# Optimization experiments

Hardware: AMD Instinct MI355X
Metric: run time of the kernel (lower is better)

The kernel has to match this reference:

```python
import jax, jax.numpy as jnp
import numpy as np

L = 256  # hardcoded heatmap size in the original module
EPS = 1e-6
SIGMA = 1.0 / 3.0
BOX_T = 0.5
MASK_T = 0.1


def _gen_mask(Yp):
    """Faithful vectorized version of get_box_pos + make_heatmap for one [L,L] map."""
    M = jnp.where(Yp > BOX_T, Yp, 0.0)
    rows = jnp.sum(M, axis=1) > 0  # scan over rows (dim 0)
    cols = jnp.sum(M, axis=0) > 0  # scan over cols (dim 1)
    left = jnp.argmax(rows)                 # first nonzero row
    right = jnp.argmax(rows[::-1])          # offset of last nonzero row from the end
    up = jnp.argmax(cols)                   # first nonzero col
    down = jnp.argmax(cols[::-1])           # offset of last nonzero col from the end
    x_r = (right - left) // 2
    y_r = (down - up) // 2
    gt0 = (left + x_r).astype(jnp.float32)  # compared against coord0 = column index y
    gt1 = (up + y_r).astype(jnp.float32)    # compared against coord1 = row index x
    # make_heatmap: heatmap[x, y, :] = [y, x]
    ys = jnp.arange(L, dtype=jnp.float32)[None, :]  # coord0 over columns
    xs = jnp.arange(L, dtype=jnp.float32)[:, None]  # coord1 over rows
    d0 = (ys - gt0) / x_r.astype(jnp.float32)
    d1 = (xs - gt1) / y_r.astype(jnp.float32)
    h = d0 ** 4 + d1 ** 4                  # ((v^2)^2 summed over last dim)
    h = jnp.exp(-h / (2.0 * SIGMA) ** 2)
    return (h > MASK_T).astype(Yp.dtype)


def _per_sample(Yp, Yg):
    gen = _gen_mask(Yp)
    use_gt = jnp.max(Yg) > 0
    Yg_eff = jnp.where(use_gt, Yg, gen)
    positive = jnp.sum(Yg_eff * Yp)
    negative = jnp.sum((1.0 - Yg_eff) * Yp)
    return negative / (positive + EPS)


def setup_inputs() -> dict:
    key = jax.random.key(0)
    k1, k2, k3 = jax.random.split(key, 3)
    B = 512
    # predictions: background in [0, 0.4), a bright blob > 0.5 so box-finding works
    Y_pred = jax.random.uniform(k1, (B, L, L), dtype=jnp.float32) * 0.4
    blob = 0.6 + 0.4 * jax.random.uniform(k3, (B, 40, 80), dtype=jnp.float32)
    Y_pred = Y_pred.at[:, 100:140, 80:160].set(blob)
    # binary gt masks; zero out first half of batch to trigger the generated-mask branch
    Y_gt = (jax.random.uniform(k2, (B, L, L)) > 0.95).astype(jnp.float32)
    Y_gt = Y_gt.at[: B // 2].set(0.0)
    return {"Y_pred": Y_pred, "Y_gt": Y_gt}


def reference(Y_pred, Y_gt):
    ratios = jax.vmap(_per_sample)(Y_pred, Y_gt)  # [B]
    total = jnp.sum(ratios)
    N = Y_gt.shape[0]
    return jnp.where(total == 0, 0.0, jnp.log(total) / N)
```

## Files before the change

### kernel.cpp

```cpp
#include <hip/hip_runtime.h>
#include <math.h>

constexpr int L = 256;
constexpr float EPS = 1e-6f;
constexpr int SPLIT = 8;
constexpr int REC_WORDS = 8;


__device__ inline float wave_sum(float v) {
#pragma unroll
    for (int off = 32; off > 0; off >>= 1) v += __shfl_down(v, off, 64);
    return v;
}
__device__ inline int wave_min(int v) {
#pragma unroll
    for (int off = 32; off > 0; off >>= 1) v = min(v, __shfl_down(v, off, 64));
    return v;
}
__device__ inline int wave_max(int v) {
#pragma unroll
    for (int off = 32; off > 0; off >>= 1) v = max(v, __shfl_down(v, off, 64));
    return v;
}

__global__ __launch_bounds__(256) void init_kernel(unsigned* __restrict__ w, int n) {
    const int i = blockIdx.x * 256 + threadIdx.x;
    if (i < n) {
        const int k = i & 7;
        unsigned v = 0u;
        if (k == 3 || k == 5) v = 0x7FFFFFFFu;
        else if (k == 4 || k == 6) v = 0xFFFFFFFFu;
        w[i] = v;
    }
}

__global__ __launch_bounds__(256) void pass1_kernel(
    const float* __restrict__ Yp, const float* __restrict__ Yg,
    unsigned* __restrict__ recs) {
    const int b = blockIdx.x >> 3;
    const int s = blockIdx.x & 7;
    const int t = threadIdx.x;
    const float4* yp4 = (const float4*)(Yp + (size_t)b * L * L) + s * 2048;
    const float4* yg4 = (const float4*)(Yg + (size_t)b * L * L) + s * 2048;
    unsigned* rec = recs + b * REC_WORDS;

    float4 P[8], G[8];
#pragma unroll
    for (int k = 0; k < 8; ++k) P[k] = yp4[t + (k << 8)];
#pragma unroll
    for (int k = 0; k < 8; ++k) G[k] = yg4[t + (k << 8)];

    const int rowbase = s * 32 + (t >> 6);
    const int c0 = (t & 63) << 2;

    float sum_p = 0.f, sum_pg = 0.f;
    int anyg = 0;
    unsigned rowbits = 0u;
    unsigned cb0 = 0, cb1 = 0, cb2 = 0, cb3 = 0;
#pragma unroll
    for (int k = 0; k < 8; ++k) {
        const float4 p = P[k], g = G[k];
        sum_p  += (p.x + p.y) + (p.z + p.w);
        sum_pg += p.x * g.x + p.y * g.y + p.z * g.z + p.w * g.w;
        anyg |= (g.x > 0.f) | (g.y > 0.f) | (g.z > 0.f) | (g.w > 0.f);
        const unsigned bx = p.x > 0.5f, by = p.y > 0.5f,
                       bz = p.z > 0.5f, bw = p.w > 0.5f;
        rowbits |= (bx | by | bz | bw) << k;
        cb0 |= bx; cb1 |= by; cb2 |= bz; cb3 |= bw;
    }
    int minr = 0x7FFFFFFF, maxr = -1, minc = 0x7FFFFFFF, maxc = -1;
    if (rowbits) {
        minr = rowbase + 4 * __builtin_ctz(rowbits);
        maxr = rowbase + 4 * (31 - __builtin_clz(rowbits));
        const unsigned colbits = cb0 | (cb1 << 1) | (cb2 << 2) | (cb3 << 3);
        minc = c0 + __builtin_ctz(colbits);
        maxc = c0 + (31 - __builtin_clz(colbits));
    }

    const int wave = t >> 6, lane = t & 63;
    const float wsp = wave_sum(sum_p);
    const float wspg = wave_sum(sum_pg);
    const int wanyg = __any(anyg);
    const int wminr = wave_min(minr), wmaxr = wave_max(maxr);
    const int wminc = wave_min(minc), wmaxc = wave_max(maxc);

    __shared__ float sh_p[4], sh_pg[4];
    __shared__ int sh_a[4], sh_minr[4], sh_maxr[4], sh_minc[4], sh_maxc[4];
    if (lane == 0) {
        sh_p[wave] = wsp; sh_pg[wave] = wspg; sh_a[wave] = wanyg;
        sh_minr[wave] = wminr; sh_maxr[wave] = wmaxr;
        sh_minc[wave] = wminc; sh_maxc[wave] = wmaxc;
    }
    __syncthreads();
    if (t == 0) {
        float sp = 0.f, spg = 0.f;
        int a = 0, mnr = 0x7FFFFFFF, mxr = -1, mnc = 0x7FFFFFFF, mxc = -1;
#pragma unroll
        for (int i = 0; i < 4; ++i) {
            sp += sh_p[i]; spg += sh_pg[i]; a |= sh_a[i];
            mnr = min(mnr, sh_minr[i]); mxr = max(mxr, sh_maxr[i]);
            mnc = min(mnc, sh_minc[i]); mxc = max(mxc, sh_maxc[i]);
        }
        atomicAdd((float*)&rec[0], sp);
        atomicAdd((float*)&rec[1], spg);
        if (a) atomicOr(&rec[2], 1u);
        if (mxr >= 0) {
            atomicMin((int*)&rec[3], mnr);
            atomicMax((int*)&rec[4], mxr);
            atomicMin((int*)&rec[5], mnc);
            atomicMax((int*)&rec[6], mxc);
        }
    }
}

__global__ __launch_bounds__(64) void pass2_kernel(
    const float* __restrict__ Yp, const unsigned* __restrict__ recs,
    float* __restrict__ ratios) {
    const int b = blockIdx.x;
    const int lane = threadIdx.x;
    const unsigned* rec = recs + b * REC_WORDS;
    const float* yp = Yp + (size_t)b * L * L;

    const float sum_p  = ((const float*)rec)[0];
    const float sum_pg = ((const float*)rec)[1];
    const unsigned anyg = rec[2];
    const int minr = (int)rec[3], maxr = (int)rec[4];
    const int minc = (int)rec[5], maxc = (int)rec[6];

    const bool any_r = maxr >= 0, any_c = maxc >= 0;
    const int left  = any_r ? minr : 0;
    const int right = any_r ? (L - 1 - maxr) : 0;
    const int up    = any_c ? minc : 0;
    const int down  = any_c ? (L - 1 - maxc) : 0;
    const int x_r = (right - left) >> 1;
    const int y_r = (down - up) >> 1;
    const float gt0 = (float)(left + x_r);
    const float gt1 = (float)(up + y_r);

    float positive;
    if (anyg) {
        positive = sum_pg;
    } else if (x_r == 0 || y_r == 0) {
        positive = 0.f;
    } else {
        const float inv_xr = 1.f / (float)x_r;
        const float inv_yr = 1.f / (float)y_r;
        const float mx = fabsf((float)x_r) * 1.02f + 1.f;
        const float my = fabsf((float)y_r) * 1.02f + 1.f;
        const int cl = max(0, (int)floorf(gt0 - mx));
        const int ch = min(L - 1, (int)ceilf(gt0 + mx));
        const int rl = max(0, (int)floorf(gt1 - my));
        const int rh = min(L - 1, (int)ceilf(gt1 + my));
        const int W = ch - cl + 1, H = rh - rl + 1;
        float pos = 0.f;
        for (int idx = lane; idx < W * H; idx += 64) {
            const int r = rl + idx / W;
            const int c = cl + idx % W;
            float d0 = ((float)c - gt0) * inv_xr;
            float d1 = ((float)r - gt1) * inv_yr;
            d0 *= d0; d0 *= d0;
            d1 *= d1; d1 *= d1;
            const float h = __expf(-2.25f * (d0 + d1));
            if (h > 0.1f) pos += yp[r * L + c];
        }
        positive = wave_sum(pos);
    }
    if (lane == 0) ratios[b] = (sum_p - positive) / (positive + EPS);
}

__global__ __launch_bounds__(256) void finalize_kernel(
    const float* __restrict__ ratios, float* __restrict__ out, int B) {
    float v = 0.f;
    for (int i = threadIdx.x; i < B; i += 256) v += ratios[i];
    v = wave_sum(v);
    __shared__ float part[4];
    const int wave = threadIdx.x >> 6, lane = threadIdx.x & 63;
    if (lane == 0) part[wave] = v;
    __syncthreads();
    if (threadIdx.x == 0) {
        const float total = part[0] + part[1] + part[2] + part[3];
        out[0] = (total == 0.f) ? 0.f : logf(total) / (float)B;
    }
}

extern "C" void kernel_launch(void* const* d_in, const int* in_sizes, int n_in,
                              void* d_out, int out_size, void* d_ws, size_t ws_size,
                              hipStream_t stream) {
    const float* Yp = (const float*)d_in[0];
    const float* Yg = (const float*)d_in[1];
    const int B = in_sizes[0] / (L * L);
    unsigned* recs = (unsigned*)d_ws;
    float* ratios = (float*)((char*)d_ws + (size_t)B * REC_WORDS * 4);
    const int nz = B * REC_WORDS;
    init_kernel<<<(nz + 255) / 256, 256, 0, stream>>>(recs, nz);
    pass1_kernel<<<B * SPLIT, 256, 0, stream>>>(Yp, Yg, recs);
    pass2_kernel<<<B, 64, 0, stream>>>(Yp, recs, ratios);
    finalize_kernel<<<1, 256, 0, stream>>>(ratios, (float*)d_out, B);
}
```

Measured before the change: 279.2 us.

## Use half-sample blocks with software-pipelined nontemporal loads in pass1

Pass1 now launches two blocks per sample instead of eight, so each block covers 128 rows. It walks them in eight chunks and prefetches the next chunk's Yp/Yg into registers while reducing the current one. Loads use nontemporal hints and row tracking widens to a 32-bit mask. This cuts per-block atomics and launch overhead and keeps loads in flight, at the cost of fewer blocks (1024) and possibly lower occupancy or memory-level parallelism.

```diff
diff --git a/kernel.cpp b/kernel.cpp
--- a/kernel.cpp
+++ b/kernel.cpp
@@ -3,9 +3,10 @@
 
 constexpr int L = 256;
 constexpr float EPS = 1e-6f;
-constexpr int SPLIT = 8;
 constexpr int REC_WORDS = 8;
 
+
+typedef float f32x4 __attribute__((ext_vector_type(4)));
 
 __device__ inline float wave_sum(float v) {
 #pragma unroll
@@ -37,20 +38,21 @@
 __global__ __launch_bounds__(256) void pass1_kernel(
     const float* __restrict__ Yp, const float* __restrict__ Yg,
     unsigned* __restrict__ recs) {
-    const int b = blockIdx.x >> 3;
-    const int s = blockIdx.x & 7;
+    const int b = blockIdx.x >> 1;
+    const int h = blockIdx.x & 1;
     const int t = threadIdx.x;
-    const float4* yp4 = (const float4*)(Yp + (size_t)b * L * L) + s * 2048;
-    const float4* yg4 = (const float4*)(Yg + (size_t)b * L * L) + s * 2048;
+    const f32x4* yp4 = (const f32x4*)(Yp + (size_t)b * L * L) + h * 8192;
+    const f32x4* yg4 = (const f32x4*)(Yg + (size_t)b * L * L) + h * 8192;
     unsigned* rec = recs + b * REC_WORDS;
 
-    float4 P[8], G[8];
-#pragma unroll
-    for (int k = 0; k < 8; ++k) P[k] = yp4[t + (k << 8)];
-#pragma unroll
-    for (int k = 0; k < 8; ++k) G[k] = yg4[t + (k << 8)];
-
-    const int rowbase = s * 32 + (t >> 6);
+    f32x4 Pc[4], Gc[4], Pn[4], Gn[4];
+#pragma unroll
+    for (int k = 0; k < 4; ++k) {
+        Pc[k] = __builtin_nontemporal_load(yp4 + (k << 8) + t);
+        Gc[k] = __builtin_nontemporal_load(yg4 + (k << 8) + t);
+    }
+
+    const int w = t >> 6;
     const int c0 = (t & 63) << 2;
 
     float sum_p = 0.f, sum_pg = 0.f;
@@ -58,20 +60,34 @@
     unsigned rowbits = 0u;
     unsigned cb0 = 0, cb1 = 0, cb2 = 0, cb3 = 0;
 #pragma unroll
-    for (int k = 0; k < 8; ++k) {
-        const float4 p = P[k], g = G[k];
-        sum_p  += (p.x + p.y) + (p.z + p.w);
-        sum_pg += p.x * g.x + p.y * g.y + p.z * g.z + p.w * g.w;
-        anyg |= (g.x > 0.f) | (g.y > 0.f) | (g.z > 0.f) | (g.w > 0.f);
-        const unsigned bx = p.x > 0.5f, by = p.y > 0.5f,
-                       bz = p.z > 0.5f, bw = p.w > 0.5f;
-        rowbits |= (bx | by | bz | bw) << k;
-        cb0 |= bx; cb1 |= by; cb2 |= bz; cb3 |= bw;
-    }
+    for (int it = 0; it < 8; ++it) {
+        if (it < 7) {
+#pragma unroll
+            for (int k = 0; k < 4; ++k) {
+                const int off = ((it + 1) << 10) + (k << 8) + t;
+                Pn[k] = __builtin_nontemporal_load(yp4 + off);
+                Gn[k] = __builtin_nontemporal_load(yg4 + off);
+            }
+        }
+#pragma unroll
+        for (int k = 0; k < 4; ++k) {
+            const f32x4 p = Pc[k], g = Gc[k];
+            sum_p  += (p[0] + p[1]) + (p[2] + p[3]);
+            sum_pg += p[0] * g[0] + p[1] * g[1] + p[2] * g[2] + p[3] * g[3];
+            anyg |= (g[0] > 0.f) | (g[1] > 0.f) | (g[2] > 0.f) | (g[3] > 0.f);
+            const unsigned bx = p[0] > 0.5f, by = p[1] > 0.5f,
+                           bz = p[2] > 0.5f, bw = p[3] > 0.5f;
+            rowbits |= (bx | by | bz | bw) << (it * 4 + k);
+            cb0 |= bx; cb1 |= by; cb2 |= bz; cb3 |= bw;
+        }
+#pragma unroll
+        for (int k = 0; k < 4; ++k) { Pc[k] = Pn[k]; Gc[k] = Gn[k]; }
+    }
+
     int minr = 0x7FFFFFFF, maxr = -1, minc = 0x7FFFFFFF, maxc = -1;
     if (rowbits) {
-        minr = rowbase + 4 * __builtin_ctz(rowbits);
-        maxr = rowbase + 4 * (31 - __builtin_clz(rowbits));
+        minr = h * 128 + w + 4 * __builtin_ctz(rowbits);
+        maxr = h * 128 + w + 4 * (31 - __builtin_clz(rowbits));
         const unsigned colbits = cb0 | (cb1 << 1) | (cb2 << 2) | (cb3 << 3);
         minc = c0 + __builtin_ctz(colbits);
         maxc = c0 + (31 - __builtin_clz(colbits));
@@ -193,7 +209,7 @@
     float* ratios = (float*)((char*)d_ws + (size_t)B * REC_WORDS * 4);
     const int nz = B * REC_WORDS;
     init_kernel<<<(nz + 255) / 256, 256, 0, stream>>>(recs, nz);
-    pass1_kernel<<<B * SPLIT, 256, 0, stream>>>(Yp, Yg, recs);
+    pass1_kernel<<<B * 2, 256, 0, stream>>>(Yp, Yg, recs);
     pass2_kernel<<<B, 64, 0, stream>>>(Yp, recs, ratios);
     finalize_kernel<<<1, 256, 0, stream>>>(ratios, (float*)d_out, B);
 }
```

Result: faster. 262.7 us (-5.9%).
